# Kernel tuning notes

Hardware: AMD Instinct MI355X
Metric: run time of the kernel (lower is better)

Reference implementation:

```python
import jax, jax.numpy as jnp
import numpy as np

N = 50000      # nodes
E = 800000     # edges
IN_DIM = 512
OUT_DIM = 64
NUM_HEADS = 8
NEG_SLOPE = 0.2


def setup_inputs() -> dict:
    key = jax.random.key(0)
    ks = jax.random.split(key, 8)
    feat = jax.random.normal(ks[0], (N, IN_DIM), dtype=jnp.float32)
    dist = jax.random.uniform(ks[1], (E, NUM_HEADS), dtype=jnp.float32)
    src = jax.random.randint(ks[2], (E,), 0, N, dtype=jnp.int32)
    dst = jax.random.randint(ks[3], (E,), 0, N, dtype=jnp.int32)
    # learned parameters (match torch init scales loosely)
    W = jax.random.normal(ks[4], (NUM_HEADS * OUT_DIM, IN_DIM), dtype=jnp.float32) / np.sqrt(IN_DIM)
    b = jax.random.normal(ks[5], (NUM_HEADS * OUT_DIM,), dtype=jnp.float32) * 0.01
    w_att_src = jax.random.normal(ks[6], (NUM_HEADS, OUT_DIM), dtype=jnp.float32)
    w_att_dst = jax.random.normal(ks[7], (NUM_HEADS, OUT_DIM), dtype=jnp.float32)
    return {"feat": feat, "dist": dist, "src": src, "dst": dst,
            "W": W, "b": b, "w_att_src": w_att_src, "w_att_dst": w_att_dst}


def reference(feat, dist, src, dst, W, b, w_att_src, w_att_dst):
    # Linear + LeakyReLU: [N, H*D]
    h = jax.nn.leaky_relu(feat @ W.T + b, negative_slope=NEG_SLOPE)
    h = h.reshape(N, NUM_HEADS, OUT_DIM)          # [N, H, D]
    # per-node attention logits
    e_src = jnp.sum(h * w_att_src, axis=-1)        # [N, H]
    e_dst = jnp.sum(h * w_att_dst, axis=-1)        # [N, H]
    # gather onto edges (u_add_v) + LeakyReLU
    e = jax.nn.leaky_relu(e_src[src] + e_dst[dst], negative_slope=NEG_SLOPE)  # [E, H]
    # edge_softmax: segment softmax over incoming edges of each dst node
    m = jax.ops.segment_max(e, dst, num_segments=N)      # [N, H]
    ex = jnp.exp(e - m[dst])                             # [E, H]
    s = jax.ops.segment_sum(ex, dst, num_segments=N)     # [N, H]
    a = (ex / s[dst]) * dist                             # [E, H]
    # u_mul_e + sum aggregation
    msg = h[src] * a[:, :, None]                         # [E, H, D]
    out = jax.ops.segment_sum(msg, dst, num_segments=N)  # [N, H, D]
    return out.reshape(N, NUM_HEADS * OUT_DIM)
```

## Files before the change

### kernel.cpp

```cpp
#include <hip/hip_runtime.h>

#define NNODES 50000
#define NEDGES 800000
#define INDIM  512
#define OUTD   512
#define NHEADS 8

typedef float  f32x4  __attribute__((ext_vector_type(4)));
typedef __bf16 bf16x8 __attribute__((ext_vector_type(8)));

__device__ __forceinline__ float lrelu(float x) { return x > 0.f ? x : 0.2f * x; }

__global__ __launch_bounds__(256) void cvt_k(const float* __restrict__ f,
                                             __bf16* __restrict__ o, int n8)
{
    int i = blockIdx.x * 256 + threadIdx.x;
    int stride = gridDim.x * 256;
    for (; i < n8; i += stride) {
        f32x4 a = *(const f32x4*)(f + (size_t)i * 8);
        f32x4 b = *(const f32x4*)(f + (size_t)i * 8 + 4);
        bf16x8 v;
        v[0]=(__bf16)a[0]; v[1]=(__bf16)a[1]; v[2]=(__bf16)a[2]; v[3]=(__bf16)a[3];
        v[4]=(__bf16)b[0]; v[5]=(__bf16)b[1]; v[6]=(__bf16)b[2]; v[7]=(__bf16)b[3];
        *(bf16x8*)(o + (size_t)i * 8) = v;
    }
}

constexpr int BM = 128, BN = 128;

__global__ __launch_bounds__(256) void gemm_h(
    const __bf16* __restrict__ featb, const __bf16* __restrict__ Wb,
    const float* __restrict__ bias, const float* __restrict__ w_s,
    const float* __restrict__ w_d, __bf16* __restrict__ hout,
    float* __restrict__ esrc, float* __restrict__ edst,
    const int* __restrict__ dstv, int* __restrict__ deg)
{
    __shared__ __bf16 As[BM][64];
    __shared__ __bf16 Bs[BN][64];
    const int col0 = blockIdx.x * BN;
    const int row0 = blockIdx.y * BM;
    const int tid  = threadIdx.x;

    {
        int bid = blockIdx.y * gridDim.x + blockIdx.x;
        int lo = bid * 512, hi = lo + 512;
        if (hi > NEDGES) hi = NEDGES;
        for (int e = lo + tid; e < hi; e += 256)
            atomicAdd(&deg[dstv[e]], 1);
    }

    const int lane = tid & 63;
    const int w    = tid >> 6;
    const int wr   = w >> 1, wc = w & 1;
    const int lr   = lane & 15, kg = lane >> 4;

    int srcA[4], srcB[4];
    #pragma unroll
    for (int i = 0; i < 4; ++i) {
        int p = tid + 256 * i;
        int r = p >> 3, ps = p & 7, sub = ps ^ (r & 7);
        int gra = row0 + r; if (gra > NNODES - 1) gra = NNODES - 1;
        srcA[i] = gra * INDIM + sub * 8;
        srcB[i] = (col0 + r) * INDIM + sub * 8;
    }

    f32x4 acc[4][4] = {};

    for (int k0 = 0; k0 < INDIM; k0 += 64) {
        #pragma unroll
        for (int i = 0; i < 4; ++i) {
            int p = tid + 256 * i;
            __builtin_amdgcn_global_load_lds(
                (const __attribute__((address_space(1))) void*)(featb + srcA[i] + k0),
                (__attribute__((address_space(3))) void*)((char*)&As[0][0] + p * 16),
                16, 0, 0);
            __builtin_amdgcn_global_load_lds(
                (const __attribute__((address_space(1))) void*)(Wb + srcB[i] + k0),
                (__attribute__((address_space(3))) void*)((char*)&Bs[0][0] + p * 16),
                16, 0, 0);
        }
        __syncthreads();
        #pragma unroll
        for (int ks = 0; ks < 2; ++ks) {
            bf16x8 af[4], bf[4];
            const int pc = ((ks * 4 + kg) ^ (lr & 7)) * 16;
            #pragma unroll
            for (int mi = 0; mi < 4; ++mi)
                af[mi] = *(const bf16x8*)((const char*)&As[0][0] + (wr*64 + mi*16 + lr) * 128 + pc);
            #pragma unroll
            for (int ni = 0; ni < 4; ++ni)
                bf[ni] = *(const bf16x8*)((const char*)&Bs[0][0] + (wc*64 + ni*16 + lr) * 128 + pc);
            #pragma unroll
            for (int mi = 0; mi < 4; ++mi)
                #pragma unroll
                for (int ni = 0; ni < 4; ++ni)
                    acc[mi][ni] = __builtin_amdgcn_mfma_f32_16x16x32_bf16(af[mi], bf[ni], acc[mi][ni], 0, 0, 0);
        }
        __syncthreads();
    }

    float cb[4], wsv[4], wdv[4];
    #pragma unroll
    for (int ni = 0; ni < 4; ++ni) {
        int c = col0 + wc * 64 + ni * 16 + lr;
        cb[ni]  = bias[c];
        wsv[ni] = w_s[c];
        wdv[ni] = w_d[c];
    }
    const int head = (col0 + wc * 64) >> 6;
    #pragma unroll
    for (int mi = 0; mi < 4; ++mi) {
        #pragma unroll
        for (int reg = 0; reg < 4; ++reg) {
            int r = row0 + wr * 64 + mi * 16 + kg * 4 + reg;
            bool valid = r < NNODES;
            float vs = 0.f, vd = 0.f;
            #pragma unroll
            for (int ni = 0; ni < 4; ++ni) {
                int c = col0 + wc * 64 + ni * 16 + lr;
                float v = acc[mi][ni][reg] + cb[ni];
                v = lrelu(v);
                if (valid) hout[(size_t)r * OUTD + c] = (__bf16)v;
                vs += v * wsv[ni];
                vd += v * wdv[ni];
            }
            #pragma unroll
            for (int m = 1; m < 16; m <<= 1) { vs += __shfl_xor(vs, m); vd += __shfl_xor(vd, m); }
            if (valid && lr == 0) {
                esrc[r * NHEADS + head] = vs;
                edst[r * NHEADS + head] = vd;
            }
        }
    }
}

__global__ __launch_bounds__(256) void scan_bsums(const int* __restrict__ deg, int* __restrict__ bsums)
{
    __shared__ int sd[256];
    int t = threadIdx.x, base = blockIdx.x * 1024, sum = 0;
    #pragma unroll
    for (int i = 0; i < 4; ++i) { int idx = base + t * 4 + i; if (idx < NNODES) sum += deg[idx]; }
    sd[t] = sum; __syncthreads();
    for (int st = 128; st > 0; st >>= 1) { if (t < st) sd[t] += sd[t + st]; __syncthreads(); }
    if (t == 0) bsums[blockIdx.x] = sd[0];
}

__global__ void scan_partials(int* __restrict__ bsums)
{
    int l = threadIdx.x;
    int orig = (l < 49) ? bsums[l] : 0;
    int v = orig;
    #pragma unroll
    for (int d = 1; d < 64; d <<= 1) { int u = __shfl_up(v, d); if (l >= d) v += u; }
    if (l < 49) bsums[l] = v - orig;
}

__global__ __launch_bounds__(256) void scan_final(
    const int* __restrict__ deg, const int* __restrict__ bsums,
    int* __restrict__ offs, int* __restrict__ cursor)
{
    __shared__ int sd[256];
    int t = threadIdx.x, base = blockIdx.x * 1024;
    int v[4]; int sum = 0;
    #pragma unroll
    for (int i = 0; i < 4; ++i) { int idx = base + t * 4 + i; v[i] = (idx < NNODES) ? deg[idx] : 0; sum += v[i]; }
    sd[t] = sum; __syncthreads();
    int val = sum;
    for (int st = 1; st < 256; st <<= 1) {
        int add = (t >= st) ? sd[t - st] : 0;
        __syncthreads();
        val += add; sd[t] = val;
        __syncthreads();
    }
    int run = bsums[blockIdx.x] + (val - sum);
    #pragma unroll
    for (int i = 0; i < 4; ++i) {
        int idx = base + t * 4 + i;
        if (idx < NNODES) { offs[idx] = run; cursor[idx] = run; }
        run += v[i];
    }
    if (blockIdx.x == 0 && t == 0) offs[NNODES] = NEDGES;
}

__global__ void scatter_k(const int* __restrict__ dstv, const int* __restrict__ src,
                          int* __restrict__ cursor, int2* __restrict__ perm)
{
    int e = blockIdx.x * blockDim.x + threadIdx.x;
    if (e < NEDGES) {
        int pos = atomicAdd(&cursor[dstv[e]], 1);
        perm[pos] = make_int2(src[e], e);
    }
}

__global__ __launch_bounds__(256) void agg_k(
    const int* __restrict__ offs, const int2* __restrict__ perm,
    const float* __restrict__ esrc, const float* __restrict__ edst,
    const float* __restrict__ dist, const __bf16* __restrict__ hmat,
    float* __restrict__ out)
{
    int node = blockIdx.x * 4 + (threadIdx.x >> 6);
    int lane = threadIdx.x & 63;
    if (node >= NNODES) return;
    const int head = lane >> 3;
    const float edv = edst[(size_t)node * NHEADS + head];
    int beg = offs[node], end = offs[node + 1];
    float denom = 0.f;
    float acc[8] = {};

    int pos = beg;
    for (; pos + 4 <= end; pos += 4) {
        int2 a0 = perm[pos], a1 = perm[pos + 1], a2 = perm[pos + 2], a3 = perm[pos + 3];
        float es0 = esrc[(size_t)a0.x * NHEADS + head];
        float es1 = esrc[(size_t)a1.x * NHEADS + head];
        float es2 = esrc[(size_t)a2.x * NHEADS + head];
        float es3 = esrc[(size_t)a3.x * NHEADS + head];
        float di0 = dist[(size_t)a0.y * NHEADS + head];
        float di1 = dist[(size_t)a1.y * NHEADS + head];
        float di2 = dist[(size_t)a2.y * NHEADS + head];
        float di3 = dist[(size_t)a3.y * NHEADS + head];
        bf16x8 h0 = *(const bf16x8*)(hmat + (size_t)a0.x * OUTD + lane * 8);
        bf16x8 h1 = *(const bf16x8*)(hmat + (size_t)a1.x * OUTD + lane * 8);
        bf16x8 h2 = *(const bf16x8*)(hmat + (size_t)a2.x * OUTD + lane * 8);
        bf16x8 h3 = *(const bf16x8*)(hmat + (size_t)a3.x * OUTD + lane * 8);
        float ex0 = __expf(lrelu(es0 + edv));
        float ex1 = __expf(lrelu(es1 + edv));
        float ex2 = __expf(lrelu(es2 + edv));
        float ex3 = __expf(lrelu(es3 + edv));
        denom += (ex0 + ex1) + (ex2 + ex3);
        float w0 = ex0 * di0, w1 = ex1 * di1, w2 = ex2 * di2, w3 = ex3 * di3;
        #pragma unroll
        for (int j = 0; j < 8; ++j)
            acc[j] += (w0 * (float)h0[j] + w1 * (float)h1[j])
                    + (w2 * (float)h2[j] + w3 * (float)h3[j]);
    }
    for (; pos < end; ++pos) {
        int2 a0 = perm[pos];
        float es0 = esrc[(size_t)a0.x * NHEADS + head];
        float di0 = dist[(size_t)a0.y * NHEADS + head];
        bf16x8 h0 = *(const bf16x8*)(hmat + (size_t)a0.x * OUTD + lane * 8);
        float ex0 = __expf(lrelu(es0 + edv));
        denom += ex0;
        float w0 = ex0 * di0;
        #pragma unroll
        for (int j = 0; j < 8; ++j) acc[j] += w0 * (float)h0[j];
    }

    float sinv = denom > 0.f ? 1.f / denom : 0.f;
    f32x4 o0 = {acc[0] * sinv, acc[1] * sinv, acc[2] * sinv, acc[3] * sinv};
    f32x4 o1 = {acc[4] * sinv, acc[5] * sinv, acc[6] * sinv, acc[7] * sinv};
    *(f32x4*)(out + (size_t)node * OUTD + lane * 8)     = o0;
    *(f32x4*)(out + (size_t)node * OUTD + lane * 8 + 4) = o1;
}

extern "C" void kernel_launch(void* const* d_in, const int* in_sizes, int n_in,
                              void* d_out, int out_size, void* d_ws, size_t ws_size,
                              hipStream_t stream)
{
    const float* feat = (const float*)d_in[0];
    const float* dist = (const float*)d_in[1];
    const int*   src  = (const int*)d_in[2];
    const int*   dstv = (const int*)d_in[3];
    const float* W    = (const float*)d_in[4];
    const float* bias = (const float*)d_in[5];
    const float* w_s  = (const float*)d_in[6];
    const float* w_d  = (const float*)d_in[7];
    float* out = (float*)d_out;

    char* wsb = (char*)d_ws;
    size_t off = 0;
    auto alloc = [&](size_t bytes) -> char* {
        char* r = wsb + off;
        off = (off + bytes + 255) & ~(size_t)255;
        return r;
    };
    __bf16* hmat  = (__bf16*)alloc((size_t)NNODES * OUTD * 2);
    __bf16* featb = (__bf16*)alloc((size_t)NNODES * INDIM * 2);
    __bf16* Wb    = (__bf16*)alloc((size_t)OUTD * INDIM * 2);
    float*  esrc  = (float*)alloc((size_t)NNODES * NHEADS * 4);
    float*  edst  = (float*)alloc((size_t)NNODES * NHEADS * 4);
    int*    deg   = (int*)alloc((size_t)NNODES * 4);
    int*    offs  = (int*)alloc((size_t)(NNODES + 1) * 4);
    int*    cursor= (int*)alloc((size_t)NNODES * 4);
    int2*   perm  = (int2*)alloc((size_t)NEDGES * 8);
    int*    bsums = (int*)alloc(64 * 4);

    hipMemsetAsync(deg, 0, (size_t)NNODES * 4, stream);

    cvt_k<<<2048, 256, 0, stream>>>(feat, featb, NNODES * INDIM / 8);
    cvt_k<<<128, 256, 0, stream>>>(W, Wb, OUTD * INDIM / 8);

    gemm_h<<<dim3(OUTD / BN, (NNODES + BM - 1) / BM), 256, 0, stream>>>(
        featb, Wb, bias, w_s, w_d, hmat, esrc, edst, dstv, deg);

    scan_bsums<<<49, 256, 0, stream>>>(deg, bsums);
    scan_partials<<<1, 64, 0, stream>>>(bsums);
    scan_final<<<49, 256, 0, stream>>>(deg, bsums, offs, cursor);
    scatter_k<<<(NEDGES + 255) / 256, 256, 0, stream>>>(dstv, src, cursor, perm);

    agg_k<<<(NNODES + 3) / 4, 256, 0, stream>>>(offs, perm, esrc, edst, dist, hmat, out);
}
```

Baseline: 484.5 us.

## Double-buffer GEMM LDS tiles, unroll aggregation by eight, merge conversion kernels

```diff
diff --git a/kernel.cpp b/kernel.cpp
--- a/kernel.cpp
+++ b/kernel.cpp
@@ -11,18 +11,27 @@
 
 __device__ __forceinline__ float lrelu(float x) { return x > 0.f ? x : 0.2f * x; }
 
-__global__ __launch_bounds__(256) void cvt_k(const float* __restrict__ f,
-                                             __bf16* __restrict__ o, int n8)
-{
-    int i = blockIdx.x * 256 + threadIdx.x;
+__global__ __launch_bounds__(256) void cvt2_k(
+    const float* __restrict__ fa, __bf16* __restrict__ oa, int na8,
+    const float* __restrict__ fb, __bf16* __restrict__ ob, int nb8)
+{
+    int i0 = blockIdx.x * 256 + threadIdx.x;
     int stride = gridDim.x * 256;
-    for (; i < n8; i += stride) {
-        f32x4 a = *(const f32x4*)(f + (size_t)i * 8);
-        f32x4 b = *(const f32x4*)(f + (size_t)i * 8 + 4);
+    for (int i = i0; i < na8; i += stride) {
+        f32x4 a = *(const f32x4*)(fa + (size_t)i * 8);
+        f32x4 b = *(const f32x4*)(fa + (size_t)i * 8 + 4);
         bf16x8 v;
         v[0]=(__bf16)a[0]; v[1]=(__bf16)a[1]; v[2]=(__bf16)a[2]; v[3]=(__bf16)a[3];
         v[4]=(__bf16)b[0]; v[5]=(__bf16)b[1]; v[6]=(__bf16)b[2]; v[7]=(__bf16)b[3];
-        *(bf16x8*)(o + (size_t)i * 8) = v;
+        *(bf16x8*)(oa + (size_t)i * 8) = v;
+    }
+    for (int i = i0; i < nb8; i += stride) {
+        f32x4 a = *(const f32x4*)(fb + (size_t)i * 8);
+        f32x4 b = *(const f32x4*)(fb + (size_t)i * 8 + 4);
+        bf16x8 v;
+        v[0]=(__bf16)a[0]; v[1]=(__bf16)a[1]; v[2]=(__bf16)a[2]; v[3]=(__bf16)a[3];
+        v[4]=(__bf16)b[0]; v[5]=(__bf16)b[1]; v[6]=(__bf16)b[2]; v[7]=(__bf16)b[3];
+        *(bf16x8*)(ob + (size_t)i * 8) = v;
     }
 }
 
@@ -35,8 +44,8 @@
     float* __restrict__ esrc, float* __restrict__ edst,
     const int* __restrict__ dstv, int* __restrict__ deg)
 {
-    __shared__ __bf16 As[BM][64];
-    __shared__ __bf16 Bs[BN][64];
+    __shared__ __bf16 As[2][BM][64];
+    __shared__ __bf16 Bs[2][BM][64];
     const int col0 = blockIdx.x * BN;
     const int row0 = blockIdx.y * BM;
     const int tid  = threadIdx.x;
@@ -64,40 +73,52 @@
         srcB[i] = (col0 + r) * INDIM + sub * 8;
     }
 
-    f32x4 acc[4][4] = {};
-
-    for (int k0 = 0; k0 < INDIM; k0 += 64) {
+    auto stage = [&](int k0, int b) {
         #pragma unroll
         for (int i = 0; i < 4; ++i) {
             int p = tid + 256 * i;
             __builtin_amdgcn_global_load_lds(
                 (const __attribute__((address_space(1))) void*)(featb + srcA[i] + k0),
-                (__attribute__((address_space(3))) void*)((char*)&As[0][0] + p * 16),
+                (__attribute__((address_space(3))) void*)((char*)&As[b][0][0] + p * 16),
                 16, 0, 0);
             __builtin_amdgcn_global_load_lds(
                 (const __attribute__((address_space(1))) void*)(Wb + srcB[i] + k0),
-                (__attribute__((address_space(3))) void*)((char*)&Bs[0][0] + p * 16),
+                (__attribute__((address_space(3))) void*)((char*)&Bs[b][0][0] + p * 16),
                 16, 0, 0);
         }
-        __syncthreads();
+    };
+
+    f32x4 acc[4][4] = {};
+
+    auto compute = [&](int b) {
         #pragma unroll
         for (int ks = 0; ks < 2; ++ks) {
             bf16x8 af[4], bf[4];
             const int pc = ((ks * 4 + kg) ^ (lr & 7)) * 16;
             #pragma unroll
             for (int mi = 0; mi < 4; ++mi)
-                af[mi] = *(const bf16x8*)((const char*)&As[0][0] + (wr*64 + mi*16 + lr) * 128 + pc);
+                af[mi] = *(const bf16x8*)((const char*)&As[b][0][0] + (wr*64 + mi*16 + lr) * 128 + pc);
             #pragma unroll
             for (int ni = 0; ni < 4; ++ni)
-                bf[ni] = *(const bf16x8*)((const char*)&Bs[0][0] + (wc*64 + ni*16 + lr) * 128 + pc);
+                bf[ni] = *(const bf16x8*)((const char*)&Bs[b][0][0] + (wc*64 + ni*16 + lr) * 128 + pc);
             #pragma unroll
             for (int mi = 0; mi < 4; ++mi)
                 #pragma unroll
                 for (int ni = 0; ni < 4; ++ni)
                     acc[mi][ni] = __builtin_amdgcn_mfma_f32_16x16x32_bf16(af[mi], bf[ni], acc[mi][ni], 0, 0, 0);
         }
+    };
+
+    stage(0, 0);
+    __syncthreads();
+    int cur = 0;
+    for (int t = 0; t < 7; ++t) {
+        stage((t + 1) * 64, cur ^ 1);
+        compute(cur);
         __syncthreads();
-    }
+        cur ^= 1;
+    }
+    compute(cur);
 
     float cb[4], wsv[4], wdv[4];
     #pragma unroll
@@ -208,30 +229,34 @@
     float acc[8] = {};
 
     int pos = beg;
-    for (; pos + 4 <= end; pos += 4) {
-        int2 a0 = perm[pos], a1 = perm[pos + 1], a2 = perm[pos + 2], a3 = perm[pos + 3];
-        float es0 = esrc[(size_t)a0.x * NHEADS + head];
-        float es1 = esrc[(size_t)a1.x * NHEADS + head];
-        float es2 = esrc[(size_t)a2.x * NHEADS + head];
-        float es3 = esrc[(size_t)a3.x * NHEADS + head];
-        float di0 = dist[(size_t)a0.y * NHEADS + head];
-        float di1 = dist[(size_t)a1.y * NHEADS + head];
-        float di2 = dist[(size_t)a2.y * NHEADS + head];
-        float di3 = dist[(size_t)a3.y * NHEADS + head];
-        bf16x8 h0 = *(const bf16x8*)(hmat + (size_t)a0.x * OUTD + lane * 8);
-        bf16x8 h1 = *(const bf16x8*)(hmat + (size_t)a1.x * OUTD + lane * 8);
-        bf16x8 h2 = *(const bf16x8*)(hmat + (size_t)a2.x * OUTD + lane * 8);
-        bf16x8 h3 = *(const bf16x8*)(hmat + (size_t)a3.x * OUTD + lane * 8);
-        float ex0 = __expf(lrelu(es0 + edv));
-        float ex1 = __expf(lrelu(es1 + edv));
-        float ex2 = __expf(lrelu(es2 + edv));
-        float ex3 = __expf(lrelu(es3 + edv));
-        denom += (ex0 + ex1) + (ex2 + ex3);
-        float w0 = ex0 * di0, w1 = ex1 * di1, w2 = ex2 * di2, w3 = ex3 * di3;
-        #pragma unroll
-        for (int j = 0; j < 8; ++j)
-            acc[j] += (w0 * (float)h0[j] + w1 * (float)h1[j])
-                    + (w2 * (float)h2[j] + w3 * (float)h3[j]);
+    for (; pos + 8 <= end; pos += 8) {
+        int2 a[8];
+        #pragma unroll
+        for (int u = 0; u < 8; ++u) a[u] = perm[pos + u];
+        bf16x8 h[8];
+        #pragma unroll
+        for (int u = 0; u < 8; ++u)
+            h[u] = *(const bf16x8*)(hmat + (size_t)a[u].x * OUTD + lane * 8);
+        float es[8], di[8];
+        #pragma unroll
+        for (int u = 0; u < 8; ++u) es[u] = esrc[(size_t)a[u].x * NHEADS + head];
+        #pragma unroll
+        for (int u = 0; u < 8; ++u) di[u] = dist[(size_t)a[u].y * NHEADS + head];
+        float ww[8]; float dsum = 0.f;
+        #pragma unroll
+        for (int u = 0; u < 8; ++u) {
+            float ex = __expf(lrelu(es[u] + edv));
+            dsum += ex; ww[u] = ex * di[u];
+        }
+        denom += dsum;
+        #pragma unroll
+        for (int j = 0; j < 8; ++j) {
+            float s0 = ww[0]*(float)h[0][j] + ww[1]*(float)h[1][j]
+                     + ww[2]*(float)h[2][j] + ww[3]*(float)h[3][j];
+            float s1 = ww[4]*(float)h[4][j] + ww[5]*(float)h[5][j]
+                     + ww[6]*(float)h[6][j] + ww[7]*(float)h[7][j];
+            acc[j] += s0 + s1;
+        }
     }
     for (; pos < end; ++pos) {
         int2 a0 = perm[pos];
@@ -286,8 +311,8 @@
 
     hipMemsetAsync(deg, 0, (size_t)NNODES * 4, stream);
 
-    cvt_k<<<2048, 256, 0, stream>>>(feat, featb, NNODES * INDIM / 8);
-    cvt_k<<<128, 256, 0, stream>>>(W, Wb, OUTD * INDIM / 8);
+    cvt2_k<<<2048, 256, 0, stream>>>(feat, featb, NNODES * INDIM / 8,
+                                     W, Wb, OUTD * INDIM / 8);
 
     gemm_h<<<dim3(OUTD / BN, (NNODES + BM - 1) / BM), 256, 0, stream>>>(
         featb, Wb, bias, w_s, w_d, hmat, esrc, edst, dstv, deg);
```

Result: no change. 489.7 us (+1.1%).
